# Optimization experiments

Hardware: AMD Instinct MI355X
Metric: run time of the kernel (lower is better)

The kernel has to match this reference:

```python
import jax, jax.numpy as jnp
import numpy as np

N = 169343
EPS = 1e-5


def gcn_norm(edge_index, n):
    """GCN normalization with self-loops: returns per-edge norm and per-node self-loop norm."""
    dst = edge_index[1]
    deg = jnp.ones((n,), jnp.float32).at[dst].add(1.0)  # in-degree + self loop
    dinv = jax.lax.rsqrt(deg)
    edge_norm = dinv[edge_index[0]] * dinv[dst]          # [E]
    self_norm = 1.0 / deg                                 # deg^-1/2 * deg^-1/2
    return edge_norm, self_norm


def gcn_conv(x, W, b, edge_index, edge_norm, self_norm):
    h = x @ W                                             # [N, out]
    msg = h[edge_index[0]] * edge_norm[:, None]           # gather + scale, [E, out]
    agg = jax.ops.segment_sum(msg, edge_index[1], num_segments=N)
    return agg + h * self_norm[:, None] + b


def batch_norm(x, gamma, beta, mean, var):
    return (x - mean) * jax.lax.rsqrt(var + EPS) * gamma + beta


def setup_inputs() -> dict:
    key = jax.random.key(0)
    ks = jax.random.split(key, 12)
    E = 2400000
    d_in, d_h, d_out = 128, 256, 40
    inp = {
        "x": jax.random.normal(ks[0], (N, d_in), jnp.float32),
        "edge_index": jax.random.randint(ks[1], (2, E), 0, N, jnp.int64),
        "W1": jax.random.normal(ks[2], (d_in, d_h), jnp.float32) / np.sqrt(d_in),
        "b1": jnp.zeros((d_h,), jnp.float32),
        "g1": 1.0 + 0.1 * jax.random.normal(ks[3], (d_h,), jnp.float32),
        "beta1": 0.1 * jax.random.normal(ks[4], (d_h,), jnp.float32),
        "m1": 0.1 * jax.random.normal(ks[5], (d_h,), jnp.float32),
        "v1": jnp.ones((d_h,), jnp.float32),
        "W2": jax.random.normal(ks[6], (d_h, d_h), jnp.float32) / np.sqrt(d_h),
        "b2": jnp.zeros((d_h,), jnp.float32),
        "g2": 1.0 + 0.1 * jax.random.normal(ks[7], (d_h,), jnp.float32),
        "beta2": 0.1 * jax.random.normal(ks[8], (d_h,), jnp.float32),
        "m2": 0.1 * jax.random.normal(ks[9], (d_h,), jnp.float32),
        "v2": jnp.ones((d_h,), jnp.float32),
        "W3": jax.random.normal(ks[10], (d_h, d_out), jnp.float32) / np.sqrt(d_h),
        "b3": jnp.zeros((d_out,), jnp.float32),
    }
    return inp


def reference(x, edge_index, W1, b1, g1, beta1, m1, v1, W2, b2, g2, beta2, m2, v2, W3, b3):
    # eval mode: BN uses running stats, dropout is identity
    edge_norm, self_norm = gcn_norm(edge_index, N)
    h = gcn_conv(x, W1, b1, edge_index, edge_norm, self_norm)
    h = jax.nn.relu(batch_norm(h, g1, beta1, m1, v1))
    h = gcn_conv(h, W2, b2, edge_index, edge_norm, self_norm)
    h = jax.nn.relu(batch_norm(h, g2, beta2, m2, v2))
    node_embeddings = h
    out = gcn_conv(h, W3, b3, edge_index, edge_norm, self_norm)
    out = jax.nn.log_softmax(out, axis=-1)
    return out, node_embeddings
```

## Files before the change

### kernel.cpp

```cpp
#include <hip/hip_runtime.h>
#include <math.h>

#define EPSV 1e-5f
#define NBMAX 680

typedef __attribute__((ext_vector_type(8))) short bf16x8;
typedef __attribute__((ext_vector_type(4))) float floatx4;

__device__ __forceinline__ unsigned short f32_to_bf16(float f) {
    unsigned int u = __float_as_uint(f);
    unsigned int r = (u + 0x7fffu + ((u >> 16) & 1u)) >> 16;
    return (unsigned short)r;
}
__device__ __forceinline__ float bf16_lo(unsigned int u) { return __uint_as_float(u << 16); }
__device__ __forceinline__ float bf16_hi(unsigned int u) { return __uint_as_float(u & 0xffff0000u); }


__global__ __launch_bounds__(256) void zero_int_kernel(int* __restrict__ p, int n) {
    int i = blockIdx.x * 256 + threadIdx.x;
    if (i < n) p[i] = 0;
}

__global__ __launch_bounds__(256) void bucket_hist_kernel(const int* __restrict__ ei,
                                                          int* __restrict__ hist,
                                                          int* __restrict__ btot,
                                                          int E, int nb) {
    __shared__ int lh[NBMAX];
    int t = threadIdx.x;
    for (int i = t; i < nb; i += 256) lh[i] = 0;
    __syncthreads();
    int chunk = (E + 255) >> 8;
    int beg = blockIdx.x * chunk;
    int end = min(beg + chunk, E);
    for (int e = beg + t; e < end; e += 256) {
        int d = ei[E + e];
        atomicAdd(&lh[d >> 8], 1);
    }
    __syncthreads();
    for (int i = t; i < nb; i += 256) {
        int v = lh[i];
        hist[i * 256 + blockIdx.x] = v;
        if (v) atomicAdd(&btot[i], v);
    }
}

__global__ __launch_bounds__(256) void bucket_offsets_kernel(const int* __restrict__ btot,
                                                             int* __restrict__ hist,
                                                             int* __restrict__ bbase, int E) {
    __shared__ int red[256];
    __shared__ int sa[256], sb[256];
    int b = blockIdx.x, t = threadIdx.x;
    int s = 0;
    for (int i = t; i < b; i += 256) s += btot[i];
    red[t] = s;
    __syncthreads();
    for (int off = 128; off > 0; off >>= 1) {
        if (t < off) red[t] += red[t + off];
        __syncthreads();
    }
    int mybase = red[0];
    if (t == 0) {
        bbase[b] = mybase;
        if (b == gridDim.x - 1) bbase[gridDim.x] = E;
    }
    int orig = hist[b * 256 + t];
    sa[t] = orig;
    __syncthreads();
    int* sp = sa; int* dp = sb;
    for (int off = 1; off < 256; off <<= 1) {
        int x = sp[t] + (t >= off ? sp[t - off] : 0);
        dp[t] = x;
        __syncthreads();
        int* q = sp; sp = dp; dp = q;
    }
    hist[b * 256 + t] = mybase + sp[t] - orig;
}

__global__ __launch_bounds__(256) void bin_kernel(const int* __restrict__ ei,
                                                  const int* __restrict__ hist,
                                                  unsigned int* __restrict__ tmp,
                                                  int E, int nb) {
    __shared__ int cur[NBMAX];
    int t = threadIdx.x;
    for (int i = t; i < nb; i += 256) cur[i] = hist[i * 256 + blockIdx.x];
    __syncthreads();
    int chunk = (E + 255) >> 8;
    int beg = blockIdx.x * chunk;
    int end = min(beg + chunk, E);
    for (int e = beg + t; e < end; e += 256) {
        int s = ei[e];
        int d = ei[E + e];
        int pos = atomicAdd(&cur[d >> 8], 1);
        tmp[pos] = ((unsigned int)(d & 255) << 24) | (unsigned int)s;
    }
}

__global__ __launch_bounds__(256) void bucket_sort_kernel(const unsigned int* __restrict__ tmp,
                                                          const int* __restrict__ bbase,
                                                          int* __restrict__ rowptr,
                                                          unsigned int* __restrict__ csr,
                                                          float* __restrict__ dinv,
                                                          float* __restrict__ selfnorm,
                                                          unsigned char* __restrict__ deg8,
                                                          int n, int E) {
    __shared__ int cnt[256];
    __shared__ int sa[256], sb[256];
    int b = blockIdx.x, t = threadIdx.x;
    int node0 = b << 8;
    int nn = min(256, n - node0);
    int ebeg = bbase[b], eend = bbase[b + 1];
    cnt[t] = 0;
    __syncthreads();
    for (int e = ebeg + t; e < eend; e += 256) {
        unsigned int v = tmp[e];
        atomicAdd(&cnt[v >> 24], 1);
    }
    __syncthreads();
    sa[t] = cnt[t];
    __syncthreads();
    int* sp = sa; int* dp = sb;
    for (int off = 1; off < 256; off <<= 1) {
        int x = sp[t] + (t >= off ? sp[t - off] : 0);
        dp[t] = x;
        __syncthreads();
        int* q = sp; sp = dp; dp = q;
    }
    int excl = sp[t] - cnt[t];
    if (t < nn) {
        rowptr[node0 + t] = ebeg + excl;
        float df = (float)(cnt[t] + 1);
        dinv[node0 + t] = rsqrtf(df);
        selfnorm[node0 + t] = 1.0f / df;
        deg8[node0 + t] = (unsigned char)(cnt[t] > 255 ? 255 : cnt[t]);
    }
    if (b == gridDim.x - 1 && t == 0) rowptr[n] = E;
    dp[t] = ebeg + excl;
    __syncthreads();
    for (int e = ebeg + t; e < eend; e += 256) {
        unsigned int v = tmp[e];
        int lpos = atomicAdd(&dp[v >> 24], 1);
        csr[lpos] = v & 0xFFFFFFu;
    }
}

__global__ __launch_bounds__(256) void csr_pack_kernel(unsigned int* __restrict__ csr,
                                                       const unsigned char* __restrict__ deg8,
                                                       int E) {
    int e = blockIdx.x * 256 + threadIdx.x;
    if (e < E) {
        unsigned int s = csr[e];
        csr[e] = s | ((unsigned int)deg8[s] << 24);
    }
}


__global__ __launch_bounds__(256) void cast_bf16_kernel(const float* __restrict__ in,
                                                        unsigned short* __restrict__ out, int n4) {
    int i = blockIdx.x * 256 + threadIdx.x;
    if (i < n4) {
        float4 f = ((const float4*)in)[i];
        ushort4 o;
        o.x = f32_to_bf16(f.x); o.y = f32_to_bf16(f.y);
        o.z = f32_to_bf16(f.z); o.w = f32_to_bf16(f.w);
        ((ushort4*)out)[i] = o;
    }
}

__global__ __launch_bounds__(256) void cast_transpose_kernel(const float* __restrict__ in,
                                                             unsigned short* __restrict__ out,
                                                             int K, int M) {
    int i = blockIdx.x * 256 + threadIdx.x;
    if (i < K * M) {
        int k = i / M, m2 = i - k * M;
        out[(size_t)m2 * K + k] = f32_to_bf16(in[i]);
    }
}


__device__ __forceinline__ void acc8(float* acc, uint4 u, float wt) {
    acc[0] += wt * bf16_lo(u.x); acc[1] += wt * bf16_hi(u.x);
    acc[2] += wt * bf16_lo(u.y); acc[3] += wt * bf16_hi(u.y);
    acc[4] += wt * bf16_lo(u.z); acc[5] += wt * bf16_hi(u.z);
    acc[6] += wt * bf16_lo(u.w); acc[7] += wt * bf16_hi(u.w);
}


template <int KT>
__global__ __launch_bounds__(256, 4) void fused_agg_gemm_kernel(
    const unsigned short* __restrict__ h, const int* __restrict__ rowptr,
    const unsigned int* __restrict__ csr, const float* __restrict__ dinv,
    const float* __restrict__ selfnorm, const unsigned short* __restrict__ Wt,
    unsigned short* __restrict__ Cb, int cstride, float* __restrict__ Cf,
    const float* __restrict__ bias, const float* __restrict__ g,
    const float* __restrict__ beta, const float* __restrict__ m,
    const float* __restrict__ v, int nrows, int M) {
    const int lda = KT + 8;
    __shared__ short As[64 * (KT + 8)];
    __shared__ short Bs[64 * 40];
    int tid = threadIdx.x;
    int row0 = blockIdx.x * 64;

    {
        const int L = KT / 8;
        const int G = 256 / L;
        int sub = tid % L, grp = tid / L;
        int fb = sub * 8;
        const unsigned short* hb = h + fb;
        for (int p = 0; p < 64; p += G) {
            int r = p + grp;
            int node = row0 + r;
            uint4 ov = make_uint4(0, 0, 0, 0);
            if (node < nrows) {
                int beg = rowptr[node], end = rowptr[node + 1];
                float acc[8] = {0.f, 0.f, 0.f, 0.f, 0.f, 0.f, 0.f, 0.f};
                int e = beg;
                for (; e + 8 <= end; e += 8) {
                    unsigned int c[8];
#pragma unroll
                    for (int q = 0; q < 8; ++q) c[q] = csr[e + q];
                    uint4 u[8];
#pragma unroll
                    for (int q = 0; q < 8; ++q)
                        u[q] = *(const uint4*)(hb + (size_t)(c[q] & 0xFFFFFFu) * KT);
#pragma unroll
                    for (int q = 0; q < 8; ++q)
                        acc8(acc, u[q], rsqrtf((float)((c[q] >> 24) + 1)));
                }
                for (; e + 4 <= end; e += 4) {
                    unsigned int c0 = csr[e], c1 = csr[e + 1], c2 = csr[e + 2], c3 = csr[e + 3];
                    uint4 u0 = *(const uint4*)(hb + (size_t)(c0 & 0xFFFFFFu) * KT);
                    uint4 u1 = *(const uint4*)(hb + (size_t)(c1 & 0xFFFFFFu) * KT);
                    uint4 u2 = *(const uint4*)(hb + (size_t)(c2 & 0xFFFFFFu) * KT);
                    uint4 u3 = *(const uint4*)(hb + (size_t)(c3 & 0xFFFFFFu) * KT);
                    acc8(acc, u0, rsqrtf((float)((c0 >> 24) + 1)));
                    acc8(acc, u1, rsqrtf((float)((c1 >> 24) + 1)));
                    acc8(acc, u2, rsqrtf((float)((c2 >> 24) + 1)));
                    acc8(acc, u3, rsqrtf((float)((c3 >> 24) + 1)));
                }
                for (; e < end; ++e) {
                    unsigned int c = csr[e];
                    uint4 u = *(const uint4*)(hb + (size_t)(c & 0xFFFFFFu) * KT);
                    acc8(acc, u, rsqrtf((float)((c >> 24) + 1)));
                }
                float di = dinv[node], sn = selfnorm[node];
                uint4 us = *(const uint4*)(hb + (size_t)node * KT);
                float hs[8];
                hs[0] = bf16_lo(us.x); hs[1] = bf16_hi(us.x);
                hs[2] = bf16_lo(us.y); hs[3] = bf16_hi(us.y);
                hs[4] = bf16_lo(us.z); hs[5] = bf16_hi(us.z);
                hs[6] = bf16_lo(us.w); hs[7] = bf16_hi(us.w);
                float o[8];
#pragma unroll
                for (int j = 0; j < 8; ++j) o[j] = acc[j] * di + hs[j] * sn;
                ov.x = ((unsigned int)f32_to_bf16(o[1]) << 16) | f32_to_bf16(o[0]);
                ov.y = ((unsigned int)f32_to_bf16(o[3]) << 16) | f32_to_bf16(o[2]);
                ov.z = ((unsigned int)f32_to_bf16(o[5]) << 16) | f32_to_bf16(o[4]);
                ov.w = ((unsigned int)f32_to_bf16(o[7]) << 16) | f32_to_bf16(o[6]);
            }
            *(uint4*)(As + r * lda + fb) = ov;
        }
    }

    int wave = tid >> 6, lane = tid & 63;
    int quad = lane >> 4, l16 = lane & 15;
    int wr = (wave >> 1) * 32, wc = (wave & 1) * 32;
    int srow = tid >> 2, sseg = tid & 3;

    int MT = (M + 63) >> 6;
    for (int jt = 0; jt < MT; ++jt) {
        int col0 = jt * 64;
        floatx4 acc[2][2];
#pragma unroll
        for (int i = 0; i < 2; ++i)
#pragma unroll
            for (int j = 0; j < 2; ++j)
#pragma unroll
                for (int r = 0; r < 4; ++r) acc[i][j][r] = 0.f;

        int gc = col0 + srow;
        uint4 bv = make_uint4(0, 0, 0, 0);
        if (gc < M) bv = *(const uint4*)(Wt + (size_t)gc * KT + sseg * 8);

        for (int k0 = 0; k0 < KT; k0 += 32) {
            *(uint4*)(Bs + srow * 40 + sseg * 8) = bv;
            __syncthreads();

            if (k0 + 32 < KT) {
                bv = make_uint4(0, 0, 0, 0);
                if (gc < M) bv = *(const uint4*)(Wt + (size_t)gc * KT + k0 + 32 + sseg * 8);
            }

            bf16x8 af[2], bfr[2];
#pragma unroll
            for (int i = 0; i < 2; ++i)
                af[i] = *(const bf16x8*)(As + (wr + i * 16 + l16) * lda + k0 + quad * 8);
#pragma unroll
            for (int j = 0; j < 2; ++j)
                bfr[j] = *(const bf16x8*)(Bs + (wc + j * 16 + l16) * 40 + quad * 8);

#pragma unroll
            for (int i = 0; i < 2; ++i)
#pragma unroll
                for (int j = 0; j < 2; ++j)
                    acc[i][j] = __builtin_amdgcn_mfma_f32_16x16x32_bf16(af[i], bfr[j], acc[i][j], 0, 0, 0);
            __syncthreads();
        }

        float sc[2], sh[2];
#pragma unroll
        for (int j = 0; j < 2; ++j) {
            int col = col0 + wc + j * 16 + l16;
            if (bias && col < M) {
                float s = g[col] * rsqrtf(v[col] + EPSV);
                sc[j] = s;
                sh[j] = (bias[col] - m[col]) * s + beta[col];
            } else {
                sc[j] = 1.f; sh[j] = 0.f;
            }
        }

#pragma unroll
        for (int i = 0; i < 2; ++i) {
#pragma unroll
            for (int r = 0; r < 4; ++r) {
                int row = row0 + wr + i * 16 + quad * 4 + r;
                if (row >= nrows) continue;
#pragma unroll
                for (int j = 0; j < 2; ++j) {
                    int col = col0 + wc + j * 16 + l16;
                    if (col < M) {
                        float val = acc[i][j][r];
                        if (bias) val = fmaxf(val * sc[j] + sh[j], 0.f);
                        if (Cb) Cb[(size_t)row * cstride + col] = f32_to_bf16(val);
                        if (Cf) Cf[(size_t)row * M + col] = val;
                    }
                }
            }
        }
    }
}


__global__ __launch_bounds__(256) void gemm_bf16_kernel(
    const unsigned short* __restrict__ A, const unsigned short* __restrict__ Wt,
    unsigned short* __restrict__ Cb, int cstride, float* __restrict__ Cf,
    const float* __restrict__ bias, const float* __restrict__ g,
    const float* __restrict__ beta, const float* __restrict__ m,
    const float* __restrict__ v, int nrows, int K, int M) {
    __shared__ short As[64 * 264];
    __shared__ short Bs[64 * 40];
    int tid = threadIdx.x;
    int wave = tid >> 6, lane = tid & 63;
    int quad = lane >> 4, l16 = lane & 15;
    int wr = (wave >> 1) * 32, wc = (wave & 1) * 32;
    int row0 = blockIdx.x * 64;
    int lda = K + 8;

    int srow = tid >> 2, sseg = tid & 3;

    {
        int gr = row0 + srow;
        for (int k0 = 0; k0 < K; k0 += 32) {
            uint4 av = make_uint4(0, 0, 0, 0);
            if (gr < nrows) av = *(const uint4*)(A + (size_t)gr * K + k0 + sseg * 8);
            *(uint4*)(As + srow * lda + k0 + sseg * 8) = av;
        }
    }

    int MT = (M + 63) >> 6;
    for (int jt = 0; jt < MT; ++jt) {
        int col0 = jt * 64;
        floatx4 acc[2][2];
#pragma unroll
        for (int i = 0; i < 2; ++i)
#pragma unroll
            for (int j = 0; j < 2; ++j)
#pragma unroll
                for (int r = 0; r < 4; ++r) acc[i][j][r] = 0.f;

        int gc = col0 + srow;
        uint4 bv = make_uint4(0, 0, 0, 0);
        if (gc < M) bv = *(const uint4*)(Wt + (size_t)gc * K + sseg * 8);

        for (int k0 = 0; k0 < K; k0 += 32) {
            *(uint4*)(Bs + srow * 40 + sseg * 8) = bv;
            __syncthreads();

            if (k0 + 32 < K) {
                bv = make_uint4(0, 0, 0, 0);
                if (gc < M) bv = *(const uint4*)(Wt + (size_t)gc * K + k0 + 32 + sseg * 8);
            }

            bf16x8 af[2], bfr[2];
#pragma unroll
            for (int i = 0; i < 2; ++i)
                af[i] = *(const bf16x8*)(As + (wr + i * 16 + l16) * lda + k0 + quad * 8);
#pragma unroll
            for (int j = 0; j < 2; ++j)
                bfr[j] = *(const bf16x8*)(Bs + (wc + j * 16 + l16) * 40 + quad * 8);

#pragma unroll
            for (int i = 0; i < 2; ++i)
#pragma unroll
                for (int j = 0; j < 2; ++j)
                    acc[i][j] = __builtin_amdgcn_mfma_f32_16x16x32_bf16(af[i], bfr[j], acc[i][j], 0, 0, 0);
            __syncthreads();
        }

        float sc[2], sh[2];
#pragma unroll
        for (int j = 0; j < 2; ++j) {
            int col = col0 + wc + j * 16 + l16;
            if (bias && col < M) {
                float s = g[col] * rsqrtf(v[col] + EPSV);
                sc[j] = s;
                sh[j] = (bias[col] - m[col]) * s + beta[col];
            } else {
                sc[j] = 1.f; sh[j] = 0.f;
            }
        }

#pragma unroll
        for (int i = 0; i < 2; ++i) {
#pragma unroll
            for (int r = 0; r < 4; ++r) {
                int row = row0 + wr + i * 16 + quad * 4 + r;
                if (row >= nrows) continue;
#pragma unroll
                for (int j = 0; j < 2; ++j) {
                    int col = col0 + wc + j * 16 + l16;
                    if (col < M) {
                        float val = acc[i][j][r];
                        if (bias) val = fmaxf(val * sc[j] + sh[j], 0.f);
                        if (Cb) Cb[(size_t)row * cstride + col] = f32_to_bf16(val);
                        if (Cf) Cf[(size_t)row * M + col] = val;
                    }
                }
            }
        }
    }
}


__global__ __launch_bounds__(256) void agg3_lsm_kernel(const unsigned short* __restrict__ h3,
                                                       const int* __restrict__ rowptr,
                                                       const unsigned int* __restrict__ csr,
                                                       const float* __restrict__ dinv,
                                                       const float* __restrict__ selfnorm,
                                                       const float* __restrict__ b3,
                                                       float* __restrict__ out, int n) {
    int node = (blockIdx.x * 256 + threadIdx.x) >> 6;
    int lane = threadIdx.x & 63;
    if (node >= n) return;
    int sub = lane & 15, grp = lane >> 4;
    int beg = rowptr[node], end = rowptr[node + 1];
    const unsigned short* hb = h3 + sub * 4;

    float acc[4] = {0.f, 0.f, 0.f, 0.f};
    int e = beg + grp;
    for (; e + 4 < end; e += 8) {
        unsigned int c0 = csr[e], c1 = csr[e + 4];
        float w0 = rsqrtf((float)((c0 >> 24) + 1));
        float w1 = rsqrtf((float)((c1 >> 24) + 1));
        uint2 u0 = *(const uint2*)(hb + (size_t)(c0 & 0xFFFFFFu) * 64);
        uint2 u1 = *(const uint2*)(hb + (size_t)(c1 & 0xFFFFFFu) * 64);
        acc[0] += w0 * bf16_lo(u0.x); acc[1] += w0 * bf16_hi(u0.x);
        acc[2] += w0 * bf16_lo(u0.y); acc[3] += w0 * bf16_hi(u0.y);
        acc[0] += w1 * bf16_lo(u1.x); acc[1] += w1 * bf16_hi(u1.x);
        acc[2] += w1 * bf16_lo(u1.y); acc[3] += w1 * bf16_hi(u1.y);
    }
    for (; e < end; e += 4) {
        unsigned int c = csr[e];
        float w = rsqrtf((float)((c >> 24) + 1));
        uint2 u = *(const uint2*)(hb + (size_t)(c & 0xFFFFFFu) * 64);
        acc[0] += w * bf16_lo(u.x); acc[1] += w * bf16_hi(u.x);
        acc[2] += w * bf16_lo(u.y); acc[3] += w * bf16_hi(u.y);
    }
#pragma unroll
    for (int j = 0; j < 4; ++j) {
        acc[j] += __shfl_xor(acc[j], 16, 64);
        acc[j] += __shfl_xor(acc[j], 32, 64);
    }
    float di = dinv[node], sn = selfnorm[node];
    uint2 us = *(const uint2*)(h3 + (size_t)node * 64 + sub * 4);
    float self4[4] = {bf16_lo(us.x), bf16_hi(us.x), bf16_lo(us.y), bf16_hi(us.y)};
    int f0 = sub * 4;
    float z[4];
#pragma unroll
    for (int j = 0; j < 4; ++j) {
        int f = f0 + j;
        int fc = f < 40 ? f : 0;
        float val = acc[j] * di + self4[j] * sn + b3[fc];
        z[j] = (f < 40) ? val : -INFINITY;
    }
    float mx = fmaxf(fmaxf(z[0], z[1]), fmaxf(z[2], z[3]));
#pragma unroll
    for (int off = 1; off < 16; off <<= 1) mx = fmaxf(mx, __shfl_xor(mx, off, 64));
    float se = expf(z[0] - mx) + expf(z[1] - mx) + expf(z[2] - mx) + expf(z[3] - mx);
#pragma unroll
    for (int off = 1; off < 16; off <<= 1) se += __shfl_xor(se, off, 64);
    float lse = logf(se);
    if (grp == 0 && sub < 10) {
        float4 o = make_float4(z[0] - mx - lse, z[1] - mx - lse, z[2] - mx - lse, z[3] - mx - lse);
        *(float4*)(out + (size_t)node * 40 + f0) = o;
    }
}


extern "C" void kernel_launch(void* const* d_in, const int* in_sizes, int n_in,
                              void* d_out, int out_size, void* d_ws, size_t ws_size,
                              hipStream_t stream) {
    const float* x  = (const float*)d_in[0];
    const int* ei   = (const int*)d_in[1];
    const float* W1 = (const float*)d_in[2];
    const float* b1 = (const float*)d_in[3];
    const float* g1 = (const float*)d_in[4];
    const float* be1 = (const float*)d_in[5];
    const float* m1 = (const float*)d_in[6];
    const float* v1 = (const float*)d_in[7];
    const float* W2 = (const float*)d_in[8];
    const float* b2 = (const float*)d_in[9];
    const float* g2 = (const float*)d_in[10];
    const float* be2 = (const float*)d_in[11];
    const float* m2 = (const float*)d_in[12];
    const float* v2 = (const float*)d_in[13];
    const float* W3 = (const float*)d_in[14];
    const float* b3 = (const float*)d_in[15];

    const int N = in_sizes[0] / 128;
    const int E = in_sizes[1] / 2;
    const int nb = (N + 255) >> 8;

    float* out_lsm = (float*)d_out;
    float* out_emb = (float*)d_out + (size_t)N * 40;

    char* ws = (char*)d_ws;
    size_t off = 0;
    auto carve = [&](size_t bytes) -> void* {
        void* p = ws + off;
        off = (off + bytes + 255) & ~(size_t)255;
        return p;
    };
    int* hist     = (int*)carve((size_t)nb * 256 * 4);
    int* btot     = (int*)carve((size_t)nb * 4);
    int* bbase    = (int*)carve((size_t)(nb + 1) * 4);
    int* rowptr   = (int*)carve((size_t)(N + 1) * 4);
    unsigned int* csr = (unsigned int*)carve((size_t)E * 4);
    float* dinv     = (float*)carve((size_t)N * 4);
    float* selfnorm = (float*)carve((size_t)N * 4);
    unsigned char* deg8 = (unsigned char*)carve((size_t)N);
    unsigned short* W1t = (unsigned short*)carve((size_t)256 * 128 * 2);
    unsigned short* W2t = (unsigned short*)carve((size_t)256 * 256 * 2);
    unsigned short* W3t = (unsigned short*)carve((size_t)40 * 256 * 2);
    unsigned short* P1 = (unsigned short*)carve((size_t)N * 256 * 2);
    unsigned short* P2 = (unsigned short*)carve((size_t)N * 256 * 2);
    (void)ws_size; (void)n_in; (void)out_size;

    unsigned short* xbf = P1;
    unsigned short* y1  = P2;
    unsigned short* y2  = P1;
    unsigned short* h3  = P2;
    unsigned int* tmp = (unsigned int*)P2;

    dim3 blk(256);

    hipLaunchKernelGGL(zero_int_kernel, dim3((nb + 255) / 256), blk, 0, stream, btot, nb);
    hipLaunchKernelGGL(bucket_hist_kernel, dim3(256), blk, 0, stream, ei, hist, btot, E, nb);
    hipLaunchKernelGGL(bucket_offsets_kernel, dim3(nb), blk, 0, stream, btot, hist, bbase, E);
    hipLaunchKernelGGL(bin_kernel, dim3(256), blk, 0, stream, ei, hist, tmp, E, nb);
    hipLaunchKernelGGL(bucket_sort_kernel, dim3(nb), blk, 0, stream, tmp, bbase, rowptr, csr,
                       dinv, selfnorm, deg8, N, E);
    hipLaunchKernelGGL(csr_pack_kernel, dim3((E + 255) / 256), blk, 0, stream, csr, deg8, E);

    int xn4 = N * 128 / 4;
    hipLaunchKernelGGL(cast_bf16_kernel, dim3((xn4 + 255) / 256), blk, 0, stream, x, xbf, xn4);
    hipLaunchKernelGGL(cast_transpose_kernel, dim3((128 * 256 + 255) / 256), blk, 0, stream,
                       W1, W1t, 128, 256);
    hipLaunchKernelGGL(cast_transpose_kernel, dim3((256 * 256 + 255) / 256), blk, 0, stream,
                       W2, W2t, 256, 256);
    hipLaunchKernelGGL(cast_transpose_kernel, dim3((256 * 40 + 255) / 256), blk, 0, stream,
                       W3, W3t, 256, 40);

    dim3 ggrid((N + 63) / 64);

    hipLaunchKernelGGL(HIP_KERNEL_NAME(fused_agg_gemm_kernel<128>), ggrid, blk, 0, stream,
                       xbf, rowptr, csr, dinv, selfnorm, W1t, y1, 256,
                       (float*)nullptr, b1, g1, be1, m1, v1, N, 256);
    hipLaunchKernelGGL(HIP_KERNEL_NAME(fused_agg_gemm_kernel<256>), ggrid, blk, 0, stream,
                       y1, rowptr, csr, dinv, selfnorm, W2t, y2, 256,
                       out_emb, b2, g2, be2, m2, v2, N, 256);
    hipLaunchKernelGGL(gemm_bf16_kernel, ggrid, blk, 0, stream, y2, W3t, h3, 64,
                       (float*)nullptr, (const float*)nullptr, (const float*)nullptr,
                       (const float*)nullptr, (const float*)nullptr, (const float*)nullptr,
                       N, 256, 40);
    hipLaunchKernelGGL(agg3_lsm_kernel, dim3((N + 3) / 4), blk, 0, stream, h3, rowptr, csr,
                       dinv, selfnorm, b3, out_lsm, N);
}
```

Baseline: 871.9 us.

## Fuse layer-3 projection GEMM into layer-2 aggregate-GEMM epilogue

The second fused aggregation+GEMM kernel now stages each 64x64 post-BN/ReLU output tile in shared memory and immediately multiplies it by the matching slice of W3, accumulating the 40-wide layer-3 projection in registers. The separate gemm_bf16 kernel and the bf16 write and re-read of the 256-wide layer-2 activations are removed. This adds an extra barrier and extra MFMA work per column tile, direct global loads of W3, and more shared memory and registers, which may lower occupancy. The weight cast-transpose kernel is also changed to write coalesced and read strided.

```diff
diff --git a/kernel.cpp b/kernel.cpp
--- a/kernel.cpp
+++ b/kernel.cpp
@@ -171,8 +171,8 @@
                                                              int K, int M) {
     int i = blockIdx.x * 256 + threadIdx.x;
     if (i < K * M) {
-        int k = i / M, m2 = i - k * M;
-        out[(size_t)m2 * K + k] = f32_to_bf16(in[i]);
+        int m2 = i / K, k = i - m2 * K;
+        out[i] = f32_to_bf16(in[(size_t)k * M + m2]);
     }
 }
 
@@ -185,7 +185,7 @@
 }
 
 
-template <int KT>
+template <int KT, bool FUSE3>
 __global__ __launch_bounds__(256, 4) void fused_agg_gemm_kernel(
     const unsigned short* __restrict__ h, const int* __restrict__ rowptr,
     const unsigned int* __restrict__ csr, const float* __restrict__ dinv,
@@ -193,10 +193,12 @@
     unsigned short* __restrict__ Cb, int cstride, float* __restrict__ Cf,
     const float* __restrict__ bias, const float* __restrict__ g,
     const float* __restrict__ beta, const float* __restrict__ m,
-    const float* __restrict__ v, int nrows, int M) {
+    const float* __restrict__ v, const unsigned short* __restrict__ W3t,
+    unsigned short* __restrict__ H3, int nrows, int M) {
     const int lda = KT + 8;
     __shared__ short As[64 * (KT + 8)];
     __shared__ short Bs[64 * 40];
+    __shared__ short Ys[FUSE3 ? 64 * 68 : 1];
     int tid = threadIdx.x;
     int row0 = blockIdx.x * 64;
 
@@ -266,6 +268,14 @@
     int wr = (wave >> 1) * 32, wc = (wave & 1) * 32;
     int srow = tid >> 2, sseg = tid & 3;
 
+    floatx4 acc3[3];
+    if constexpr (FUSE3) {
+#pragma unroll
+        for (int jj = 0; jj < 3; ++jj)
+#pragma unroll
+            for (int r = 0; r < 4; ++r) acc3[jj][r] = 0.f;
+    }
+
     int MT = (M + 63) >> 6;
     for (int jt = 0; jt < MT; ++jt) {
         int col0 = jt * 64;
@@ -331,111 +341,43 @@
                     if (col < M) {
                         float val = acc[i][j][r];
                         if (bias) val = fmaxf(val * sc[j] + sh[j], 0.f);
-                        if (Cb) Cb[(size_t)row * cstride + col] = f32_to_bf16(val);
+                        unsigned short hv = f32_to_bf16(val);
+                        if constexpr (FUSE3)
+                            Ys[(wr + i * 16 + quad * 4 + r) * 68 + wc + j * 16 + l16] = (short)hv;
+                        if (Cb) Cb[(size_t)row * cstride + col] = hv;
                         if (Cf) Cf[(size_t)row * M + col] = val;
                     }
                 }
             }
         }
-    }
-}
-
-
-__global__ __launch_bounds__(256) void gemm_bf16_kernel(
-    const unsigned short* __restrict__ A, const unsigned short* __restrict__ Wt,
-    unsigned short* __restrict__ Cb, int cstride, float* __restrict__ Cf,
-    const float* __restrict__ bias, const float* __restrict__ g,
-    const float* __restrict__ beta, const float* __restrict__ m,
-    const float* __restrict__ v, int nrows, int K, int M) {
-    __shared__ short As[64 * 264];
-    __shared__ short Bs[64 * 40];
-    int tid = threadIdx.x;
-    int wave = tid >> 6, lane = tid & 63;
-    int quad = lane >> 4, l16 = lane & 15;
-    int wr = (wave >> 1) * 32, wc = (wave & 1) * 32;
-    int row0 = blockIdx.x * 64;
-    int lda = K + 8;
-
-    int srow = tid >> 2, sseg = tid & 3;
-
-    {
-        int gr = row0 + srow;
-        for (int k0 = 0; k0 < K; k0 += 32) {
-            uint4 av = make_uint4(0, 0, 0, 0);
-            if (gr < nrows) av = *(const uint4*)(A + (size_t)gr * K + k0 + sseg * 8);
-            *(uint4*)(As + srow * lda + k0 + sseg * 8) = av;
-        }
-    }
-
-    int MT = (M + 63) >> 6;
-    for (int jt = 0; jt < MT; ++jt) {
-        int col0 = jt * 64;
-        floatx4 acc[2][2];
-#pragma unroll
-        for (int i = 0; i < 2; ++i)
-#pragma unroll
-            for (int j = 0; j < 2; ++j)
-#pragma unroll
-                for (int r = 0; r < 4; ++r) acc[i][j][r] = 0.f;
-
-        int gc = col0 + srow;
-        uint4 bv = make_uint4(0, 0, 0, 0);
-        if (gc < M) bv = *(const uint4*)(Wt + (size_t)gc * K + sseg * 8);
-
-        for (int k0 = 0; k0 < K; k0 += 32) {
-            *(uint4*)(Bs + srow * 40 + sseg * 8) = bv;
+
+        if constexpr (FUSE3) {
             __syncthreads();
-
-            if (k0 + 32 < K) {
-                bv = make_uint4(0, 0, 0, 0);
-                if (gc < M) bv = *(const uint4*)(Wt + (size_t)gc * K + k0 + 32 + sseg * 8);
-            }
-
-            bf16x8 af[2], bfr[2];
-#pragma unroll
-            for (int i = 0; i < 2; ++i)
-                af[i] = *(const bf16x8*)(As + (wr + i * 16 + l16) * lda + k0 + quad * 8);
-#pragma unroll
-            for (int j = 0; j < 2; ++j)
-                bfr[j] = *(const bf16x8*)(Bs + (wc + j * 16 + l16) * 40 + quad * 8);
-
-#pragma unroll
-            for (int i = 0; i < 2; ++i)
-#pragma unroll
-                for (int j = 0; j < 2; ++j)
-                    acc[i][j] = __builtin_amdgcn_mfma_f32_16x16x32_bf16(af[i], bfr[j], acc[i][j], 0, 0, 0);
-            __syncthreads();
-        }
-
-        float sc[2], sh[2];
-#pragma unroll
-        for (int j = 0; j < 2; ++j) {
-            int col = col0 + wc + j * 16 + l16;
-            if (bias && col < M) {
-                float s = g[col] * rsqrtf(v[col] + EPSV);
-                sc[j] = s;
-                sh[j] = (bias[col] - m[col]) * s + beta[col];
-            } else {
-                sc[j] = 1.f; sh[j] = 0.f;
+            const bf16x8 bz = {0, 0, 0, 0, 0, 0, 0, 0};
+#pragma unroll
+            for (int ks = 0; ks < 2; ++ks) {
+                bf16x8 af3 = *(const bf16x8*)(Ys + (wave * 16 + l16) * 68 + ks * 32 + quad * 8);
+#pragma unroll
+                for (int jj = 0; jj < 3; ++jj) {
+                    int c3 = jj * 16 + l16;
+                    bf16x8 bf3 = bz;
+                    if (c3 < 40)
+                        bf3 = *(const bf16x8*)(W3t + (size_t)c3 * 256 + jt * 64 + ks * 32 + quad * 8);
+                    acc3[jj] = __builtin_amdgcn_mfma_f32_16x16x32_bf16(af3, bf3, acc3[jj], 0, 0, 0);
+                }
             }
         }
-
-#pragma unroll
-        for (int i = 0; i < 2; ++i) {
+    }
+
+    if constexpr (FUSE3) {
+#pragma unroll
+        for (int jj = 0; jj < 3; ++jj) {
 #pragma unroll
             for (int r = 0; r < 4; ++r) {
-                int row = row0 + wr + i * 16 + quad * 4 + r;
-                if (row >= nrows) continue;
-#pragma unroll
-                for (int j = 0; j < 2; ++j) {
-                    int col = col0 + wc + j * 16 + l16;
-                    if (col < M) {
-                        float val = acc[i][j][r];
-                        if (bias) val = fmaxf(val * sc[j] + sh[j], 0.f);
-                        if (Cb) Cb[(size_t)row * cstride + col] = f32_to_bf16(val);
-                        if (Cf) Cf[(size_t)row * M + col] = val;
-                    }
-                }
+                int row = row0 + wave * 16 + quad * 4 + r;
+                int col = jj * 16 + l16;
+                if (row < nrows && col < 40)
+                    H3[(size_t)row * 64 + col] = f32_to_bf16(acc3[jj][r]);
             }
         }
     }
@@ -558,8 +500,7 @@
 
     unsigned short* xbf = P1;
     unsigned short* y1  = P2;
-    unsigned short* y2  = P1;
-    unsigned short* h3  = P2;
+    unsigned short* h3  = P1;
     unsigned int* tmp = (unsigned int*)P2;
 
     dim3 blk(256);
@@ -583,16 +524,13 @@
 
     dim3 ggrid((N + 63) / 64);
 
-    hipLaunchKernelGGL(HIP_KERNEL_NAME(fused_agg_gemm_kernel<128>), ggrid, blk, 0, stream,
+    hipLaunchKernelGGL(HIP_KERNEL_NAME(fused_agg_gemm_kernel<128, false>), ggrid, blk, 0, stream,
                        xbf, rowptr, csr, dinv, selfnorm, W1t, y1, 256,
-                       (float*)nullptr, b1, g1, be1, m1, v1, N, 256);
-    hipLaunchKernelGGL(HIP_KERNEL_NAME(fused_agg_gemm_kernel<256>), ggrid, blk, 0, stream,
-                       y1, rowptr, csr, dinv, selfnorm, W2t, y2, 256,
-                       out_emb, b2, g2, be2, m2, v2, N, 256);
-    hipLaunchKernelGGL(gemm_bf16_kernel, ggrid, blk, 0, stream, y2, W3t, h3, 64,
-                       (float*)nullptr, (const float*)nullptr, (const float*)nullptr,
-                       (const float*)nullptr, (const float*)nullptr, (const float*)nullptr,
-                       N, 256, 40);
+                       (float*)nullptr, b1, g1, be1, m1, v1,
+                       (const unsigned short*)nullptr, (unsigned short*)nullptr, N, 256);
+    hipLaunchKernelGGL(HIP_KERNEL_NAME(fused_agg_gemm_kernel<256, true>), ggrid, blk, 0, stream,
+                       y1, rowptr, csr, dinv, selfnorm, W2t, (unsigned short*)nullptr, 256,
+                       out_emb, b2, g2, be2, m2, v2, W3t, h3, N, 256);
     hipLaunchKernelGGL(agg3_lsm_kernel, dim3((N + 3) / 4), blk, 0, stream, h3, rowptr, csr,
                        dinv, selfnorm, b3, out_lsm, N);
 }
```

Result: no change. 861.4 us (-1.2%).
